# Performance work log

Measured on AMD Instinct MI355X. Metric: run time of the kernel, lower is better.

The kernel has to match this reference:

```python
import jax, jax.numpy as jnp
import numpy as np

N = 100000
E = 1600000
D_IN = 128
H = 128
C = 3
EPS_BN = 1e-5
EPS_LN = 1e-5


def _gcn_conv(x, W, b, src, dst, ew, n):
    # PyG GCNConv: x' = D^{-1/2} (A + I) D^{-1/2} (x W) + b, self-loop weight 1
    x = x @ W
    loop = jnp.arange(n)
    src2 = jnp.concatenate([src, loop])
    dst2 = jnp.concatenate([dst, loop])
    ew2 = jnp.concatenate([ew, jnp.ones((n,), dtype=x.dtype)])
    deg = jax.ops.segment_sum(ew2, dst2, num_segments=n)
    dinv = jnp.where(deg > 0, jax.lax.rsqrt(jnp.maximum(deg, 1e-12)), 0.0)
    norm = dinv[src2] * ew2 * dinv[dst2]  # [E+N]
    msgs = x[src2] * norm[:, None]        # [E+N, H] gathered messages
    out = jax.ops.segment_sum(msgs, dst2, num_segments=n)
    return out + b


def setup_inputs() -> dict:
    key = jax.random.key(0)
    ks = jax.random.split(key, 16)
    def lin(k, i, o):
        s = 1.0 / np.sqrt(i)
        k1, k2 = jax.random.split(k)
        return (jax.random.uniform(k1, (i, o), jnp.float32, -s, s),
                jax.random.uniform(k2, (o,), jnp.float32, -s, s))
    x = jax.random.normal(ks[0], (N, D_IN), jnp.float32)
    edge_index = jax.random.randint(ks[1], (2, E), 0, N, jnp.int64)
    edge_attr = jax.random.uniform(ks[2], (E, 1), jnp.float32)
    W_pre, b_pre = lin(ks[3], D_IN, H)
    W1, b1 = lin(ks[4], H, H)
    W2, b2 = lin(ks[5], H, H)
    Wc1, bc1 = lin(ks[6], H, H)
    Wc2, bc2 = lin(ks[7], H, C)
    return {
        "x": x, "edge_index": edge_index, "edge_attr": edge_attr,
        "W_pre": W_pre, "b_pre": b_pre,
        "bn_gamma": jnp.ones((H,), jnp.float32), "bn_beta": jnp.zeros((H,), jnp.float32),
        "bn_mean": jnp.zeros((H,), jnp.float32), "bn_var": jnp.ones((H,), jnp.float32),
        "W1": W1, "b1": b1, "W2": W2, "b2": b2,
        "Wc1": Wc1, "bc1": bc1,
        "ln_g": jnp.ones((H,), jnp.float32), "ln_b": jnp.zeros((H,), jnp.float32),
        "Wc2": Wc2, "bc2": bc2,
    }


def reference(x, edge_index, edge_attr, W_pre, b_pre, bn_gamma, bn_beta, bn_mean, bn_var,
              W1, b1, W2, b2, Wc1, bc1, ln_g, ln_b, Wc2, bc2):
    src, dst = edge_index[0], edge_index[1]
    ew = edge_attr.squeeze()
    n = x.shape[0]
    # input_preprocess: Linear -> BatchNorm1d (eval: running stats) -> ReLU (dropout=identity)
    h = x @ W_pre + b_pre
    h = (h - bn_mean) * jax.lax.rsqrt(bn_var + EPS_BN) * bn_gamma + bn_beta
    h = jax.nn.relu(h)
    residual = h
    # conv layer 1 (+ ReLU, dropout identity in eval)
    h = jax.nn.relu(_gcn_conv(h, W1, b1, src, dst, ew, n))
    # conv layer 2 (last: no activation)
    h = _gcn_conv(h, W2, b2, src, dst, ew, n)
    h = h + residual  # shapes match
    # classifier: Linear -> LayerNorm -> ReLU -> (dropout) -> Linear
    z = h @ Wc1 + bc1
    mu = jnp.mean(z, axis=-1, keepdims=True)
    var = jnp.mean((z - mu) ** 2, axis=-1, keepdims=True)
    z = (z - mu) * jax.lax.rsqrt(var + EPS_LN) * ln_g + ln_b
    z = jax.nn.relu(z)
    return z @ Wc2 + bc2
```

## Files before the change

kernel.cpp:

```cpp
#include <hip/hip_runtime.h>
#include <hip/hip_bf16.h>

typedef __bf16 bf16_t;
typedef bf16_t bf16x8 __attribute__((ext_vector_type(8)));
typedef bf16_t bf16x4 __attribute__((ext_vector_type(4)));
typedef float f32x4 __attribute__((ext_vector_type(4)));
typedef float f32x2 __attribute__((ext_vector_type(2)));

#define EPS_BN 1e-5f
#define EPS_LN 1e-5f
#define SLOTS 32
#define WSCALE 32767.f
#define WINV (1.f / 32767.f)
#define RNODES 448
#define OV_CAP 16384
#define OVA_CAP 65536

__device__ __forceinline__ float blo(unsigned u) { return __uint_as_float(u << 16); }
__device__ __forceinline__ float bhi(unsigned u) { return __uint_as_float(u & 0xFFFF0000u); }
__device__ __forceinline__ f32x2 f8lo(unsigned u) { return __builtin_amdgcn_cvt_pk_f32_fp8((int)u, false); }
__device__ __forceinline__ f32x2 f8hi(unsigned u) { return __builtin_amdgcn_cvt_pk_f32_fp8((int)u, true); }


__global__ void prepK(const float* __restrict__ W0, const float* __restrict__ W1,
                      const float* __restrict__ W2, const float* __restrict__ W3,
                      bf16_t* __restrict__ WT, int* __restrict__ bCnt,
                      int* __restrict__ ovCnt, int* __restrict__ ovACnt, int n) {
    int flat = blockIdx.x * 256 + threadIdx.x;
    if (flat == 0) { *ovCnt = 0; *ovACnt = 0; }
    if (flat < 4096) bCnt[flat] = 0;
    if (flat < 65536) {
        int which = flat >> 14, r = flat & 16383;
        const float* W = (which == 0) ? W0 : (which == 1) ? W1 : (which == 2) ? W2 : W3;
        int i = r >> 7, o = r & 127;
        WT[which * 128 * 136 + o * 136 + i] = (bf16_t)W[r];
    }
}


__global__ __launch_bounds__(256) void binK(
    const int* __restrict__ ei, const float* __restrict__ ea,
    uint2* __restrict__ bbuf, int* __restrict__ bCnt,
    uint2* __restrict__ ovA, int* __restrict__ ovACnt,
    int E, int cap, int nbuck)
{
    __shared__ int lcnt[256];
    __shared__ int gbase[256];
    int tid = threadIdx.x;
    if (tid < nbuck) lcnt[tid] = 0;
    __syncthreads();

    int e0 = blockIdx.x * 4096 + tid;
    int d[16]; unsigned pk[16]; int p[16];
#pragma unroll
    for (int k = 0; k < 16; ++k) {
        int e = e0 + k * 256;
        p[k] = -1;
        if (e < E) {
            d[k] = ei[E + e];
            int s = ei[e];
            unsigned wq = __float2uint_rn(ea[e] * WSCALE);
            pk[k] = ((unsigned)s << 15) | wq;
            p[k] = atomicAdd(&lcnt[(unsigned)d[k] / RNODES], 1);
        }
    }
    __syncthreads();
    if (tid < nbuck) gbase[tid] = atomicAdd(&bCnt[tid * 16], lcnt[tid]);
    __syncthreads();
#pragma unroll
    for (int k = 0; k < 16; ++k) {
        if (p[k] >= 0) {
            int b = (unsigned)d[k] / RNODES;
            int idx = gbase[b] + p[k];
            if (idx < cap) {
                bbuf[(size_t)b * cap + idx] = make_uint2((unsigned)d[k], pk[k]);
            } else {
                int o = atomicAdd(ovACnt, 1);
                if (o < OVA_CAP) ovA[o] = make_uint2((unsigned)d[k], pk[k]);
            }
        }
    }
}


__global__ __launch_bounds__(256) void buildK(
    const uint2* __restrict__ bbuf, const int* __restrict__ bCnt,
    const uint2* __restrict__ ovA, const int* __restrict__ ovACnt,
    unsigned* __restrict__ slots, int* __restrict__ cnt,
    float* __restrict__ dinv, uint2* __restrict__ ov, int* __restrict__ ovCnt,
    int cap, int n)
{
    __shared__ unsigned slotsL[RNODES * 32];
    __shared__ int cntL[RNODES];
    __shared__ float wsumL[RNODES];
    int tid = threadIdx.x;
    int base = blockIdx.x * RNODES;

    for (int j = tid; j < RNODES; j += 256) { cntL[j] = 0; wsumL[j] = 0.f; }
    __syncthreads();

    int nb = min(bCnt[blockIdx.x * 16], cap);
    const uint2* buf = bbuf + (size_t)blockIdx.x * cap;
    for (int i = tid; i < nb; i += 256) {
        uint2 u = buf[i];
        int local = (int)u.x - base;
        int pos = atomicAdd(&cntL[local], 1);
        atomicAdd(&wsumL[local], (float)(u.y & 32767u) * WINV);
        if (pos < SLOTS) {
            slotsL[local * 32 + pos] = u.y;
        } else {
            int o = atomicAdd(ovCnt, 1);
            if (o < OV_CAP) ov[o] = u;
        }
    }
    int no = min(*ovACnt, OVA_CAP);
    for (int k = tid; k < no; k += 256) {
        uint2 u = ovA[k];
        int local = (int)u.x - base;
        if (local >= 0 && local < RNODES) {
            int pos = atomicAdd(&cntL[local], 1);
            atomicAdd(&wsumL[local], (float)(u.y & 32767u) * WINV);
            if (pos < SLOTS) {
                slotsL[local * 32 + pos] = u.y;
            } else {
                int o = atomicAdd(ovCnt, 1);
                if (o < OV_CAP) ov[o] = u;
            }
        }
    }
    __syncthreads();

    for (int j = tid; j < RNODES; j += 256) {
        int node = base + j;
        if (node < n) {
            int c = cntL[j];
            int cm = min(c, SLOTS);
            int c8 = (cm + 7) & ~7;
            for (int k2 = cm; k2 < c8; ++k2) slotsL[j * 32 + k2] = (unsigned)node << 15;
            cnt[node] = c;
            dinv[node] = rsqrtf(fmaxf(1.f + wsumL[j], 1e-12f));
        }
    }
    __syncthreads();

    int vnodes = min(n - base, RNODES);
    if (vnodes <= 0) return;
    const uint4* sl4 = (const uint4*)slotsL;
    uint4* sg4 = (uint4*)(slots + ((size_t)base << 5));
    int lim = vnodes * 8;
    for (int i = tid; i < lim; i += 256) sg4[i] = sl4[i];
}


template <int MODE, typename AT>
__global__ __launch_bounds__(256) void gemm128K(
    const AT* __restrict__ A, const bf16_t* __restrict__ WT,
    bf16_t* __restrict__ outb, unsigned* __restrict__ out8,
    const float* __restrict__ colBias,
    const float* __restrict__ bnMean, const float* __restrict__ bnVar,
    const float* __restrict__ bnG, const float* __restrict__ bnB,
    const float* __restrict__ dinv, int nrows)
{
    __shared__ __align__(16) bf16_t Bs[128 * 136];
    int tid = threadIdx.x;
    int rb = blockIdx.x * 64;

    {
        const uint4* src = (const uint4*)WT;
        uint4* dst = (uint4*)Bs;
        if (MODE == 1) {
            for (int i = tid; i < 128 * 17; i += 256) {
                int row = i / 17, k = i - row * 17;
                int so = ((row & 15) << 3) | (row >> 4);
                dst[row * 17 + k] = src[so * 17 + k];
            }
        } else {
            for (int i = tid; i < 128 * 17; i += 256) dst[i] = src[i];
        }
    }

    int lane = tid & 63;
    int wid = tid >> 6;
    int m = lane & 15, q = lane >> 4;
    int myRow = rb + wid * 16 + m;
    int rowL = min(myRow, nrows - 1);

    bf16x8 af[4];
    if constexpr (sizeof(AT) == 4) {
#pragma unroll
        for (int kk = 0; kk < 4; ++kk) {
            float4 v0 = ((const float4*)A)[rowL * 32 + q * 2 + kk * 8];
            float4 v1 = ((const float4*)A)[rowL * 32 + q * 2 + kk * 8 + 1];
            bf16x8 w8;
            w8[0] = (bf16_t)v0.x; w8[1] = (bf16_t)v0.y; w8[2] = (bf16_t)v0.z; w8[3] = (bf16_t)v0.w;
            w8[4] = (bf16_t)v1.x; w8[5] = (bf16_t)v1.y; w8[6] = (bf16_t)v1.z; w8[7] = (bf16_t)v1.w;
            af[kk] = w8;
        }
    } else {
#pragma unroll
        for (int kk = 0; kk < 4; ++kk)
            af[kk] = ((const bf16x8*)A)[rowL * 16 + q + kk * 4];
    }

    __syncthreads();

    f32x4 acc[8];
#pragma unroll
    for (int c = 0; c < 8; ++c) acc[c] = (f32x4){0.f, 0.f, 0.f, 0.f};

#pragma unroll
    for (int kk = 0; kk < 4; ++kk) {
#pragma unroll
        for (int c = 0; c < 8; ++c) {
            bf16x8 bfr = *(const bf16x8*)&Bs[(c * 16 + m) * 136 + q * 8 + kk * 32];
            acc[c] = __builtin_amdgcn_mfma_f32_16x16x32_bf16(af[kk], bfr, acc[c], 0, 0, 0);
        }
    }

    int r0 = rb + wid * 16 + q * 4;
    if (MODE == 1) {
        float dv[4];
#pragma unroll
        for (int i = 0; i < 4; ++i) dv[i] = (r0 + i < nrows) ? dinv[r0 + i] : 0.f;
#pragma unroll
        for (int i = 0; i < 4; ++i) {
            int r = r0 + i;
            if (r < nrows) {
                float v0 = acc[0][i] * dv[i], v1 = acc[1][i] * dv[i];
                float v2 = acc[2][i] * dv[i], v3 = acc[3][i] * dv[i];
                float v4 = acc[4][i] * dv[i], v5 = acc[5][i] * dv[i];
                float v6 = acc[6][i] * dv[i], v7 = acc[7][i] * dv[i];
                int lo = __builtin_amdgcn_cvt_pk_fp8_f32(v0, v1, 0, false);
                lo = __builtin_amdgcn_cvt_pk_fp8_f32(v2, v3, lo, true);
                int hi = __builtin_amdgcn_cvt_pk_fp8_f32(v4, v5, 0, false);
                hi = __builtin_amdgcn_cvt_pk_fp8_f32(v6, v7, hi, true);
                ((uint2*)out8)[(r << 4) | m] = make_uint2((unsigned)lo, (unsigned)hi);
            }
        }
    } else {
#pragma unroll
        for (int c = 0; c < 8; ++c) {
            int j = c * 16 + m;
            float cb = colBias[j];
            float rs = rsqrtf(bnVar[j] + EPS_BN);
            float scale = bnG[j] * rs;
            float shift = bnB[j] - bnMean[j] * scale;
#pragma unroll
            for (int i = 0; i < 4; ++i) {
                int r = r0 + i;
                if (r < nrows) {
                    float v = (acc[c][i] + cb) * scale + shift;
                    outb[r * 128 + j] = (bf16_t)fmaxf(v, 0.f);
                }
            }
        }
    }
}


template <int RELU, int RES>
__global__ __launch_bounds__(256) void aggK(
    const uint4* __restrict__ ts16, const unsigned* __restrict__ slots,
    const int* __restrict__ cnt, const float* __restrict__ dinv,
    const float4* __restrict__ bias, const uint4* __restrict__ residual,
    uint4* __restrict__ out,
    const uint2* __restrict__ ov, const int* __restrict__ ovCnt, int n)
{
    int tid = threadIdx.x;
    int node = blockIdx.x * 8 + (tid >> 5);
    int hl = tid & 31;
    int hb = tid & 32;
    if (node >= n) return;
    int slot = hl >> 3;
    int f = hl & 7;
    int nb = node << 5;

    int c8 = (min(cnt[node], SLOTS) + 7) & ~7;
    unsigned my = slots[nb | hl];
    float myw = (float)(my & 32767u) * WINV;
    int myoff = (int)(my >> 15) << 3;

    f32x2 acc[8];
#pragma unroll
    for (int k = 0; k < 8; ++k) acc[k] = (f32x2){0.f, 0.f};

    if (slot == 1) {
        uint4 su = ts16[(node << 3) + f];
        acc[0] += f8lo(su.x); acc[1] += f8hi(su.x);
        acc[2] += f8lo(su.y); acc[3] += f8hi(su.y);
        acc[4] += f8lo(su.z); acc[5] += f8hi(su.z);
        acc[6] += f8lo(su.w); acc[7] += f8hi(su.w);
    }

    for (int j = 0; j < c8; j += 8) {
        int s0 = hb + j + slot;
        int s1 = s0 + 4;
        int o0 = __shfl(myoff, s0);
        int o1 = __shfl(myoff, s1);
        float w0 = __shfl(myw, s0);
        float w1 = __shfl(myw, s1);
        uint4 u0 = ts16[o0 + f];
        uint4 u1 = ts16[o1 + f];
        f32x2 W0 = (f32x2){w0, w0}, W1 = (f32x2){w1, w1};
        acc[0] += W0 * f8lo(u0.x) + W1 * f8lo(u1.x);
        acc[1] += W0 * f8hi(u0.x) + W1 * f8hi(u1.x);
        acc[2] += W0 * f8lo(u0.y) + W1 * f8lo(u1.y);
        acc[3] += W0 * f8hi(u0.y) + W1 * f8hi(u1.y);
        acc[4] += W0 * f8lo(u0.z) + W1 * f8lo(u1.z);
        acc[5] += W0 * f8hi(u0.z) + W1 * f8hi(u1.z);
        acc[6] += W0 * f8lo(u0.w) + W1 * f8lo(u1.w);
        acc[7] += W0 * f8hi(u0.w) + W1 * f8hi(u1.w);
    }

    int no = min(*ovCnt, OV_CAP);
    for (int k = 0; k < no; ++k) {
        uint2 o = ov[k];
        if ((int)o.x == node && slot == 0) {
            uint4 u = ts16[((int)(o.y >> 15) << 3) + f];
            float w = (float)(o.y & 32767u) * WINV;
            f32x2 W = (f32x2){w, w};
            acc[0] += W * f8lo(u.x); acc[1] += W * f8hi(u.x);
            acc[2] += W * f8lo(u.y); acc[3] += W * f8hi(u.y);
            acc[4] += W * f8lo(u.z); acc[5] += W * f8hi(u.z);
            acc[6] += W * f8lo(u.w); acc[7] += W * f8hi(u.w);
        }
    }

#pragma unroll
    for (int k = 0; k < 8; ++k) {
        f32x2 t;
        t.x = __shfl_xor(acc[k].x, 8);  t.y = __shfl_xor(acc[k].y, 8);
        acc[k] += t;
        t.x = __shfl_xor(acc[k].x, 16); t.y = __shfl_xor(acc[k].y, 16);
        acc[k] += t;
    }

    if (slot == 0) {
        float di = dinv[node];
        float r[16];
#pragma unroll
        for (int k = 0; k < 8; ++k) {
            float4 bb = bias[f * 4 + (k >> 1)];
            float b0 = (k & 1) ? bb.z : bb.x;
            float b1 = (k & 1) ? bb.w : bb.y;
            r[2 * k]     = acc[k].x * di + b0;
            r[2 * k + 1] = acc[k].y * di + b1;
        }
        if (RES) {
            uint4 q0 = residual[(node << 4) + f * 2];
            uint4 q1 = residual[(node << 4) + f * 2 + 1];
            r[0] += blo(q0.x);  r[1] += bhi(q0.x);
            r[2] += blo(q0.y);  r[3] += bhi(q0.y);
            r[4] += blo(q0.z);  r[5] += bhi(q0.z);
            r[6] += blo(q0.w);  r[7] += bhi(q0.w);
            r[8] += blo(q1.x);  r[9] += bhi(q1.x);
            r[10] += blo(q1.y); r[11] += bhi(q1.y);
            r[12] += blo(q1.z); r[13] += bhi(q1.z);
            r[14] += blo(q1.w); r[15] += bhi(q1.w);
        }
        if (RELU) {
#pragma unroll
            for (int k = 0; k < 16; ++k) r[k] = fmaxf(r[k], 0.f);
        }
        bf16x8 o0, o1;
#pragma unroll
        for (int k = 0; k < 8; ++k) { o0[k] = (bf16_t)r[k]; o1[k] = (bf16_t)r[8 + k]; }
        out[(node << 4) + f * 2]     = *(uint4*)&o0;
        out[(node << 4) + f * 2 + 1] = *(uint4*)&o1;
    }
}


__global__ __launch_bounds__(256) void classifierK(
    const bf16_t* __restrict__ A, const bf16_t* __restrict__ WT,
    const float* __restrict__ bc1, const float* __restrict__ g,
    const float* __restrict__ b, const float* __restrict__ Wc2,
    const float* __restrict__ bc2, float* __restrict__ out, int nrows)
{
    __shared__ __align__(16) bf16_t Bs[128 * 136];
    __shared__ float sB[128], sG[128], sLb[128], sW2[384];
    int tid = threadIdx.x;
    int rb = blockIdx.x * 64;

    {
        const uint4* src = (const uint4*)WT;
        uint4* dst = (uint4*)Bs;
        for (int i = tid; i < 128 * 17; i += 256) dst[i] = src[i];
    }
    if (tid < 128) { sB[tid] = bc1[tid]; sG[tid] = g[tid]; sLb[tid] = b[tid]; }
    for (int i = tid; i < 384; i += 256) sW2[i] = Wc2[i];

    int lane = tid & 63;
    int wid = tid >> 6;
    int m = lane & 15, q = lane >> 4;
    int rowL = min(rb + wid * 16 + m, nrows - 1);

    bf16x8 af[4];
#pragma unroll
    for (int kk = 0; kk < 4; ++kk)
        af[kk] = ((const bf16x8*)A)[rowL * 16 + q + kk * 4];

    __syncthreads();

    f32x4 acc[8];
#pragma unroll
    for (int c = 0; c < 8; ++c) acc[c] = (f32x4){0.f, 0.f, 0.f, 0.f};
#pragma unroll
    for (int kk = 0; kk < 4; ++kk) {
#pragma unroll
        for (int c = 0; c < 8; ++c) {
            bf16x8 bfr = *(const bf16x8*)&Bs[(c * 16 + m) * 136 + q * 8 + kk * 32];
            acc[c] = __builtin_amdgcn_mfma_f32_16x16x32_bf16(af[kk], bfr, acc[c], 0, 0, 0);
        }
    }

    int r0 = rb + wid * 16 + q * 4;
#pragma unroll
    for (int i = 0; i < 4; ++i) {
        float s1 = 0.f, s2 = 0.f;
#pragma unroll
        for (int c = 0; c < 8; ++c) {
            float z = acc[c][i] + sB[c * 16 + m];
            acc[c][i] = z;
            s1 += z; s2 += z * z;
        }
#pragma unroll
        for (int off = 1; off < 16; off <<= 1) {
            s1 += __shfl_xor(s1, off);
            s2 += __shfl_xor(s2, off);
        }
        float mu = s1 * (1.f / 128.f);
        float var = s2 * (1.f / 128.f) - mu * mu;
        float rstd = rsqrtf(var + EPS_LN);
        float p0 = 0.f, p1 = 0.f, p2 = 0.f;
#pragma unroll
        for (int c = 0; c < 8; ++c) {
            int j = c * 16 + m;
            float zn = (acc[c][i] - mu) * rstd * sG[j] + sLb[j];
            zn = fmaxf(zn, 0.f);
            p0 += zn * sW2[j * 3 + 0];
            p1 += zn * sW2[j * 3 + 1];
            p2 += zn * sW2[j * 3 + 2];
        }
#pragma unroll
        for (int off = 1; off < 16; off <<= 1) {
            p0 += __shfl_xor(p0, off);
            p1 += __shfl_xor(p1, off);
            p2 += __shfl_xor(p2, off);
        }
        int r = r0 + i;
        if (m == 0 && r < nrows) {
            out[r * 3 + 0] = p0 + bc2[0];
            out[r * 3 + 1] = p1 + bc2[1];
            out[r * 3 + 2] = p2 + bc2[2];
        }
    }
}


extern "C" void kernel_launch(void* const* d_in, const int* in_sizes, int n_in,
                              void* d_out, int out_size, void* d_ws, size_t ws_size,
                              hipStream_t stream) {
    const float* x      = (const float*)d_in[0];
    const int*   ei     = (const int*)d_in[1];
    const float* ea     = (const float*)d_in[2];
    const float* W_pre  = (const float*)d_in[3];
    const float* b_pre  = (const float*)d_in[4];
    const float* bn_g   = (const float*)d_in[5];
    const float* bn_b   = (const float*)d_in[6];
    const float* bn_m   = (const float*)d_in[7];
    const float* bn_v   = (const float*)d_in[8];
    const float* W1     = (const float*)d_in[9];
    const float* b1     = (const float*)d_in[10];
    const float* W2     = (const float*)d_in[11];
    const float* b2     = (const float*)d_in[12];
    const float* Wc1    = (const float*)d_in[13];
    const float* bc1    = (const float*)d_in[14];
    const float* ln_g   = (const float*)d_in[15];
    const float* ln_b   = (const float*)d_in[16];
    const float* Wc2    = (const float*)d_in[17];
    const float* bc2    = (const float*)d_in[18];
    float* outp = (float*)d_out;

    const int N = in_sizes[0] / 128;
    const int E = in_sizes[2];

    char* p = (char*)d_ws;
    auto alloc = [&](size_t bytes) -> void* {
        void* r = (void*)p;
        p += (bytes + 255) & ~(size_t)255;
        return r;
    };
    bf16_t*   h0    = (bf16_t*)alloc((size_t)N * 128 * 2);
    bf16_t*   bufB  = (bf16_t*)alloc((size_t)N * 128 * 2);
    unsigned* ts8   = (unsigned*)alloc((size_t)N * 128);
    float*    dinv  = (float*)alloc((size_t)N * 4);
    int*      cnt   = (int*)alloc((size_t)N * 4);
    int*      ovCnt = (int*)alloc(256);
    int*      ovACnt= (int*)alloc(256);
    uint2*    ov    = (uint2*)alloc((size_t)OV_CAP * 8);
    uint2*    ovA   = (uint2*)alloc((size_t)OVA_CAP * 8);
    unsigned* slots = (unsigned*)alloc((size_t)N * SLOTS * 4);
    bf16_t*   WT    = (bf16_t*)alloc((size_t)4 * 128 * 136 * 2);
    int       nbuck = (N + RNODES - 1) / RNODES;
    int       cap   = E / nbuck + 4096;
    uint2*    bbuf  = (uint2*)alloc((size_t)nbuck * cap * 8);
    int*      bCnt  = (int*)alloc(4096 * 4);

    bf16_t* WT_pre = WT + 0 * 128 * 136;
    bf16_t* WT_1   = WT + 1 * 128 * 136;
    bf16_t* WT_2   = WT + 2 * 128 * 136;
    bf16_t* WT_c1  = WT + 3 * 128 * 136;

    int gG = (N + 63) / 64;
    int gH = (N + 7) / 8;
    int gP = (max(N, 65536) + 255) / 256;
    int gBin = (E + 4095) / 4096;

    prepK<<<gP, 256, 0, stream>>>(W_pre, W1, W2, Wc1, WT, bCnt, ovCnt, ovACnt, N);
    binK<<<gBin, 256, 0, stream>>>(ei, ea, bbuf, bCnt, ovA, ovACnt, E, cap, nbuck);
    buildK<<<nbuck, 256, 0, stream>>>(bbuf, bCnt, ovA, ovACnt, slots, cnt, dinv, ov, ovCnt, cap, N);

    gemm128K<0, float><<<gG, 256, 0, stream>>>(x, WT_pre, h0, nullptr, b_pre, bn_m, bn_v, bn_g, bn_b, nullptr, N);
    gemm128K<1, bf16_t><<<gG, 256, 0, stream>>>(h0, WT_1, nullptr, ts8, nullptr, nullptr, nullptr, nullptr, nullptr, dinv, N);
    aggK<1, 0><<<gH, 256, 0, stream>>>((const uint4*)ts8, slots, cnt, dinv, (const float4*)b1,
                                       nullptr, (uint4*)bufB, ov, ovCnt, N);
    gemm128K<1, bf16_t><<<gG, 256, 0, stream>>>(bufB, WT_2, nullptr, ts8, nullptr, nullptr, nullptr, nullptr, nullptr, dinv, N);
    aggK<0, 1><<<gH, 256, 0, stream>>>((const uint4*)ts8, slots, cnt, dinv, (const float4*)b2,
                                       (const uint4*)h0, (uint4*)bufB, ov, ovCnt, N);
    classifierK<<<gG, 256, 0, stream>>>(bufB, WT_c1, bc1, ln_g, ln_b, Wc2, bc2, outp, N);
}
```

Baseline: 322.4 us.

## Persistent GEMM blocks and software-pipelined neighbor gathers in aggregation

The GEMM and classifier kernels become grid-stride persistent loops capped at 1024 blocks. Each block now loads the 128x128 weight tile into shared memory once and reuses it across many row groups, instead of reloading it for every 64 rows. The aggregation kernel double-buffers its neighbor gathers: it prefetches the next pair of fp8 rows and their weights before accumulating the current pair, which hides gather latency at the cost of extra registers. It also loads the self-row unconditionally and trims the prepK launch size.

```diff
diff --git a/kernel.cpp b/kernel.cpp
--- a/kernel.cpp
+++ b/kernel.cpp
@@ -25,7 +25,7 @@
 __global__ void prepK(const float* __restrict__ W0, const float* __restrict__ W1,
                       const float* __restrict__ W2, const float* __restrict__ W3,
                       bf16_t* __restrict__ WT, int* __restrict__ bCnt,
-                      int* __restrict__ ovCnt, int* __restrict__ ovACnt, int n) {
+                      int* __restrict__ ovCnt, int* __restrict__ ovACnt) {
     int flat = blockIdx.x * 256 + threadIdx.x;
     if (flat == 0) { *ovCnt = 0; *ovACnt = 0; }
     if (flat < 4096) bCnt[flat] = 0;
@@ -86,8 +86,8 @@
 __global__ __launch_bounds__(256) void buildK(
     const uint2* __restrict__ bbuf, const int* __restrict__ bCnt,
     const uint2* __restrict__ ovA, const int* __restrict__ ovACnt,
-    unsigned* __restrict__ slots, int* __restrict__ cnt,
-    float* __restrict__ dinv, uint2* __restrict__ ov, int* __restrict__ ovCnt,
+    unsigned* __restrict__ slots, int* __restrict__ cnt, float* __restrict__ dinv,
+    uint2* __restrict__ ov, int* __restrict__ ovCnt,
     int cap, int n)
 {
     __shared__ unsigned slotsL[RNODES * 32];
@@ -159,11 +159,10 @@
     const float* __restrict__ colBias,
     const float* __restrict__ bnMean, const float* __restrict__ bnVar,
     const float* __restrict__ bnG, const float* __restrict__ bnB,
-    const float* __restrict__ dinv, int nrows)
+    const float* __restrict__ dinv, int nrows, int ngroups)
 {
     __shared__ __align__(16) bf16_t Bs[128 * 136];
     int tid = threadIdx.x;
-    int rb = blockIdx.x * 64;
 
     {
         const uint4* src = (const uint4*)WT;
@@ -182,81 +181,99 @@
     int lane = tid & 63;
     int wid = tid >> 6;
     int m = lane & 15, q = lane >> 4;
-    int myRow = rb + wid * 16 + m;
-    int rowL = min(myRow, nrows - 1);
-
-    bf16x8 af[4];
-    if constexpr (sizeof(AT) == 4) {
-#pragma unroll
-        for (int kk = 0; kk < 4; ++kk) {
-            float4 v0 = ((const float4*)A)[rowL * 32 + q * 2 + kk * 8];
-            float4 v1 = ((const float4*)A)[rowL * 32 + q * 2 + kk * 8 + 1];
-            bf16x8 w8;
-            w8[0] = (bf16_t)v0.x; w8[1] = (bf16_t)v0.y; w8[2] = (bf16_t)v0.z; w8[3] = (bf16_t)v0.w;
-            w8[4] = (bf16_t)v1.x; w8[5] = (bf16_t)v1.y; w8[6] = (bf16_t)v1.z; w8[7] = (bf16_t)v1.w;
-            af[kk] = w8;
-        }
-    } else {
-#pragma unroll
-        for (int kk = 0; kk < 4; ++kk)
-            af[kk] = ((const bf16x8*)A)[rowL * 16 + q + kk * 4];
-    }
-
-    __syncthreads();
-
-    f32x4 acc[8];
-#pragma unroll
-    for (int c = 0; c < 8; ++c) acc[c] = (f32x4){0.f, 0.f, 0.f, 0.f};
-
-#pragma unroll
-    for (int kk = 0; kk < 4; ++kk) {
-#pragma unroll
-        for (int c = 0; c < 8; ++c) {
-            bf16x8 bfr = *(const bf16x8*)&Bs[(c * 16 + m) * 136 + q * 8 + kk * 32];
-            acc[c] = __builtin_amdgcn_mfma_f32_16x16x32_bf16(af[kk], bfr, acc[c], 0, 0, 0);
-        }
-    }
-
-    int r0 = rb + wid * 16 + q * 4;
-    if (MODE == 1) {
-        float dv[4];
-#pragma unroll
-        for (int i = 0; i < 4; ++i) dv[i] = (r0 + i < nrows) ? dinv[r0 + i] : 0.f;
-#pragma unroll
-        for (int i = 0; i < 4; ++i) {
-            int r = r0 + i;
-            if (r < nrows) {
-                float v0 = acc[0][i] * dv[i], v1 = acc[1][i] * dv[i];
-                float v2 = acc[2][i] * dv[i], v3 = acc[3][i] * dv[i];
-                float v4 = acc[4][i] * dv[i], v5 = acc[5][i] * dv[i];
-                float v6 = acc[6][i] * dv[i], v7 = acc[7][i] * dv[i];
-                int lo = __builtin_amdgcn_cvt_pk_fp8_f32(v0, v1, 0, false);
-                lo = __builtin_amdgcn_cvt_pk_fp8_f32(v2, v3, lo, true);
-                int hi = __builtin_amdgcn_cvt_pk_fp8_f32(v4, v5, 0, false);
-                hi = __builtin_amdgcn_cvt_pk_fp8_f32(v6, v7, hi, true);
-                ((uint2*)out8)[(r << 4) | m] = make_uint2((unsigned)lo, (unsigned)hi);
-            }
-        }
-    } else {
+
+    float cb[8], scale[8], shift[8];
+    if (MODE == 0) {
 #pragma unroll
         for (int c = 0; c < 8; ++c) {
             int j = c * 16 + m;
-            float cb = colBias[j];
+            cb[c] = colBias[j];
             float rs = rsqrtf(bnVar[j] + EPS_BN);
-            float scale = bnG[j] * rs;
-            float shift = bnB[j] - bnMean[j] * scale;
+            scale[c] = bnG[j] * rs;
+            shift[c] = bnB[j] - bnMean[j] * scale[c];
+        }
+    }
+
+    __syncthreads();
+
+    for (int g = blockIdx.x; g < ngroups; g += gridDim.x) {
+        int rb = g * 64;
+        int myRow = rb + wid * 16 + m;
+        int rowL = min(myRow, nrows - 1);
+
+        bf16x8 af[4];
+        if constexpr (sizeof(AT) == 4) {
+#pragma unroll
+            for (int kk = 0; kk < 4; ++kk) {
+                float4 v0 = ((const float4*)A)[rowL * 32 + q * 2 + kk * 8];
+                float4 v1 = ((const float4*)A)[rowL * 32 + q * 2 + kk * 8 + 1];
+                bf16x8 w8;
+                w8[0] = (bf16_t)v0.x; w8[1] = (bf16_t)v0.y; w8[2] = (bf16_t)v0.z; w8[3] = (bf16_t)v0.w;
+                w8[4] = (bf16_t)v1.x; w8[5] = (bf16_t)v1.y; w8[6] = (bf16_t)v1.z; w8[7] = (bf16_t)v1.w;
+                af[kk] = w8;
+            }
+        } else {
+#pragma unroll
+            for (int kk = 0; kk < 4; ++kk)
+                af[kk] = ((const bf16x8*)A)[rowL * 16 + q + kk * 4];
+        }
+
+        f32x4 acc[8];
+#pragma unroll
+        for (int c = 0; c < 8; ++c) acc[c] = (f32x4){0.f, 0.f, 0.f, 0.f};
+
+#pragma unroll
+        for (int kk = 0; kk < 4; ++kk) {
+#pragma unroll
+            for (int c = 0; c < 8; ++c) {
+                bf16x8 bfr = *(const bf16x8*)&Bs[(c * 16 + m) * 136 + q * 8 + kk * 32];
+                acc[c] = __builtin_amdgcn_mfma_f32_16x16x32_bf16(af[kk], bfr, acc[c], 0, 0, 0);
+            }
+        }
+
+        int r0 = rb + wid * 16 + q * 4;
+        if (MODE == 1) {
+            float dv[4];
+#pragma unroll
+            for (int i = 0; i < 4; ++i) dv[i] = (r0 + i < nrows) ? dinv[r0 + i] : 0.f;
 #pragma unroll
             for (int i = 0; i < 4; ++i) {
                 int r = r0 + i;
                 if (r < nrows) {
-                    float v = (acc[c][i] + cb) * scale + shift;
-                    outb[r * 128 + j] = (bf16_t)fmaxf(v, 0.f);
+                    float v0 = acc[0][i] * dv[i], v1 = acc[1][i] * dv[i];
+                    float v2 = acc[2][i] * dv[i], v3 = acc[3][i] * dv[i];
+                    float v4 = acc[4][i] * dv[i], v5 = acc[5][i] * dv[i];
+                    float v6 = acc[6][i] * dv[i], v7 = acc[7][i] * dv[i];
+                    int lo = __builtin_amdgcn_cvt_pk_fp8_f32(v0, v1, 0, false);
+                    lo = __builtin_amdgcn_cvt_pk_fp8_f32(v2, v3, lo, true);
+                    int hi = __builtin_amdgcn_cvt_pk_fp8_f32(v4, v5, 0, false);
+                    hi = __builtin_amdgcn_cvt_pk_fp8_f32(v6, v7, hi, true);
+                    ((uint2*)out8)[(r << 4) | m] = make_uint2((unsigned)lo, (unsigned)hi);
                 }
             }
-        }
-    }
-}
-
+        } else {
+#pragma unroll
+            for (int c = 0; c < 8; ++c) {
+#pragma unroll
+                for (int i = 0; i < 4; ++i) {
+                    int r = r0 + i;
+                    if (r < nrows) {
+                        float v = (acc[c][i] + cb[c]) * scale[c] + shift[c];
+                        outb[r * 128 + (c * 16 + m)] = (bf16_t)fmaxf(v, 0.f);
+                    }
+                }
+            }
+        }
+    }
+}
+
+
+#define ACC8(U, W) do { \
+    f32x2 Wv = (f32x2){(W), (W)}; \
+    acc[0] += Wv * f8lo((U).x); acc[1] += Wv * f8hi((U).x); \
+    acc[2] += Wv * f8lo((U).y); acc[3] += Wv * f8hi((U).y); \
+    acc[4] += Wv * f8lo((U).z); acc[5] += Wv * f8hi((U).z); \
+    acc[6] += Wv * f8lo((U).w); acc[7] += Wv * f8hi((U).w); } while (0)
 
 template <int RELU, int RES>
 __global__ __launch_bounds__(256) void aggK(
@@ -273,56 +290,57 @@
     if (node >= n) return;
     int slot = hl >> 3;
     int f = hl & 7;
-    int nb = node << 5;
 
     int c8 = (min(cnt[node], SLOTS) + 7) & ~7;
-    unsigned my = slots[nb | hl];
+    int nit = c8 >> 3;
+    unsigned my = slots[(node << 5) | hl];
     float myw = (float)(my & 32767u) * WINV;
     int myoff = (int)(my >> 15) << 3;
 
+    uint4 su = ts16[(node << 3) + f];
+
+    int s0 = hb + slot;
+    int po0 = __shfl(myoff, s0);
+    int po1 = __shfl(myoff, s0 + 4);
+    float pw0 = __shfl(myw, s0);
+    float pw1 = __shfl(myw, s0 + 4);
+    uint4 u0 = su, u1 = su;
+    if (nit > 0) { u0 = ts16[po0 + f]; u1 = ts16[po1 + f]; }
+
     f32x2 acc[8];
 #pragma unroll
     for (int k = 0; k < 8; ++k) acc[k] = (f32x2){0.f, 0.f};
 
     if (slot == 1) {
-        uint4 su = ts16[(node << 3) + f];
         acc[0] += f8lo(su.x); acc[1] += f8hi(su.x);
         acc[2] += f8lo(su.y); acc[3] += f8hi(su.y);
         acc[4] += f8lo(su.z); acc[5] += f8hi(su.z);
         acc[6] += f8lo(su.w); acc[7] += f8hi(su.w);
     }
 
-    for (int j = 0; j < c8; j += 8) {
-        int s0 = hb + j + slot;
-        int s1 = s0 + 4;
-        int o0 = __shfl(myoff, s0);
-        int o1 = __shfl(myoff, s1);
-        float w0 = __shfl(myw, s0);
-        float w1 = __shfl(myw, s1);
-        uint4 u0 = ts16[o0 + f];
-        uint4 u1 = ts16[o1 + f];
-        f32x2 W0 = (f32x2){w0, w0}, W1 = (f32x2){w1, w1};
-        acc[0] += W0 * f8lo(u0.x) + W1 * f8lo(u1.x);
-        acc[1] += W0 * f8hi(u0.x) + W1 * f8hi(u1.x);
-        acc[2] += W0 * f8lo(u0.y) + W1 * f8lo(u1.y);
-        acc[3] += W0 * f8hi(u0.y) + W1 * f8hi(u1.y);
-        acc[4] += W0 * f8lo(u0.z) + W1 * f8lo(u1.z);
-        acc[5] += W0 * f8hi(u0.z) + W1 * f8hi(u1.z);
-        acc[6] += W0 * f8lo(u0.w) + W1 * f8lo(u1.w);
-        acc[7] += W0 * f8hi(u0.w) + W1 * f8hi(u1.w);
+    for (int j = 0; j < nit; ++j) {
+        uint4 v0 = u0, v1 = u1;
+        float x0 = pw0, x1 = pw1;
+        if (j + 1 < nit) {
+            int s = hb + (j + 1) * 8 + slot;
+            int no0 = __shfl(myoff, s);
+            int no1 = __shfl(myoff, s + 4);
+            pw0 = __shfl(myw, s);
+            pw1 = __shfl(myw, s + 4);
+            u0 = ts16[no0 + f];
+            u1 = ts16[no1 + f];
+        }
+        ACC8(v0, x0);
+        ACC8(v1, x1);
     }
 
     int no = min(*ovCnt, OV_CAP);
     for (int k = 0; k < no; ++k) {
-        uint2 o = ov[k];
-        if ((int)o.x == node && slot == 0) {
-            uint4 u = ts16[((int)(o.y >> 15) << 3) + f];
-            float w = (float)(o.y & 32767u) * WINV;
-            f32x2 W = (f32x2){w, w};
-            acc[0] += W * f8lo(u.x); acc[1] += W * f8hi(u.x);
-            acc[2] += W * f8lo(u.y); acc[3] += W * f8hi(u.y);
-            acc[4] += W * f8lo(u.z); acc[5] += W * f8hi(u.z);
-            acc[6] += W * f8lo(u.w); acc[7] += W * f8hi(u.w);
+        uint2 ovk = ov[k];
+        if ((int)ovk.x == node && slot == 0) {
+            uint4 uo = ts16[((int)(ovk.y >> 15) << 3) + f];
+            float wo = (float)(ovk.y & 32767u) * WINV;
+            ACC8(uo, wo);
         }
     }
 
@@ -375,12 +393,11 @@
     const bf16_t* __restrict__ A, const bf16_t* __restrict__ WT,
     const float* __restrict__ bc1, const float* __restrict__ g,
     const float* __restrict__ b, const float* __restrict__ Wc2,
-    const float* __restrict__ bc2, float* __restrict__ out, int nrows)
+    const float* __restrict__ bc2, float* __restrict__ out, int nrows, int ngroups)
 {
     __shared__ __align__(16) bf16_t Bs[128 * 136];
     __shared__ float sB[128], sG[128], sLb[128], sW2[384];
     int tid = threadIdx.x;
-    int rb = blockIdx.x * 64;
 
     {
         const uint4* src = (const uint4*)WT;
@@ -393,66 +410,70 @@
     int lane = tid & 63;
     int wid = tid >> 6;
     int m = lane & 15, q = lane >> 4;
-    int rowL = min(rb + wid * 16 + m, nrows - 1);
-
-    bf16x8 af[4];
-#pragma unroll
-    for (int kk = 0; kk < 4; ++kk)
-        af[kk] = ((const bf16x8*)A)[rowL * 16 + q + kk * 4];
-
-    __syncthreads();
-
-    f32x4 acc[8];
-#pragma unroll
-    for (int c = 0; c < 8; ++c) acc[c] = (f32x4){0.f, 0.f, 0.f, 0.f};
-#pragma unroll
-    for (int kk = 0; kk < 4; ++kk) {
-#pragma unroll
-        for (int c = 0; c < 8; ++c) {
-            bf16x8 bfr = *(const bf16x8*)&Bs[(c * 16 + m) * 136 + q * 8 + kk * 32];
-            acc[c] = __builtin_amdgcn_mfma_f32_16x16x32_bf16(af[kk], bfr, acc[c], 0, 0, 0);
-        }
-    }
-
-    int r0 = rb + wid * 16 + q * 4;
-#pragma unroll
-    for (int i = 0; i < 4; ++i) {
-        float s1 = 0.f, s2 = 0.f;
-#pragma unroll
-        for (int c = 0; c < 8; ++c) {
-            float z = acc[c][i] + sB[c * 16 + m];
-            acc[c][i] = z;
-            s1 += z; s2 += z * z;
-        }
-#pragma unroll
-        for (int off = 1; off < 16; off <<= 1) {
-            s1 += __shfl_xor(s1, off);
-            s2 += __shfl_xor(s2, off);
-        }
-        float mu = s1 * (1.f / 128.f);
-        float var = s2 * (1.f / 128.f) - mu * mu;
-        float rstd = rsqrtf(var + EPS_LN);
-        float p0 = 0.f, p1 = 0.f, p2 = 0.f;
-#pragma unroll
-        for (int c = 0; c < 8; ++c) {
-            int j = c * 16 + m;
-            float zn = (acc[c][i] - mu) * rstd * sG[j] + sLb[j];
-            zn = fmaxf(zn, 0.f);
-            p0 += zn * sW2[j * 3 + 0];
-            p1 += zn * sW2[j * 3 + 1];
-            p2 += zn * sW2[j * 3 + 2];
-        }
-#pragma unroll
-        for (int off = 1; off < 16; off <<= 1) {
-            p0 += __shfl_xor(p0, off);
-            p1 += __shfl_xor(p1, off);
-            p2 += __shfl_xor(p2, off);
-        }
-        int r = r0 + i;
-        if (m == 0 && r < nrows) {
-            out[r * 3 + 0] = p0 + bc2[0];
-            out[r * 3 + 1] = p1 + bc2[1];
-            out[r * 3 + 2] = p2 + bc2[2];
+
+    __syncthreads();
+
+    for (int grp = blockIdx.x; grp < ngroups; grp += gridDim.x) {
+        int rb = grp * 64;
+        int rowL = min(rb + wid * 16 + m, nrows - 1);
+
+        bf16x8 af[4];
+#pragma unroll
+        for (int kk = 0; kk < 4; ++kk)
+            af[kk] = ((const bf16x8*)A)[rowL * 16 + q + kk * 4];
+
+        f32x4 acc[8];
+#pragma unroll
+        for (int c = 0; c < 8; ++c) acc[c] = (f32x4){0.f, 0.f, 0.f, 0.f};
+#pragma unroll
+        for (int kk = 0; kk < 4; ++kk) {
+#pragma unroll
+            for (int c = 0; c < 8; ++c) {
+                bf16x8 bfr = *(const bf16x8*)&Bs[(c * 16 + m) * 136 + q * 8 + kk * 32];
+                acc[c] = __builtin_amdgcn_mfma_f32_16x16x32_bf16(af[kk], bfr, acc[c], 0, 0, 0);
+            }
+        }
+
+        int r0 = rb + wid * 16 + q * 4;
+#pragma unroll
+        for (int i = 0; i < 4; ++i) {
+            float s1 = 0.f, s2 = 0.f;
+#pragma unroll
+            for (int c = 0; c < 8; ++c) {
+                float z = acc[c][i] + sB[c * 16 + m];
+                acc[c][i] = z;
+                s1 += z; s2 += z * z;
+            }
+#pragma unroll
+            for (int off = 1; off < 16; off <<= 1) {
+                s1 += __shfl_xor(s1, off);
+                s2 += __shfl_xor(s2, off);
+            }
+            float mu = s1 * (1.f / 128.f);
+            float var = s2 * (1.f / 128.f) - mu * mu;
+            float rstd = rsqrtf(var + EPS_LN);
+            float p0 = 0.f, p1 = 0.f, p2 = 0.f;
+#pragma unroll
+            for (int c = 0; c < 8; ++c) {
+                int j = c * 16 + m;
+                float zn = (acc[c][i] - mu) * rstd * sG[j] + sLb[j];
+                zn = fmaxf(zn, 0.f);
+                p0 += zn * sW2[j * 3 + 0];
+                p1 += zn * sW2[j * 3 + 1];
+                p2 += zn * sW2[j * 3 + 2];
+            }
+#pragma unroll
+            for (int off = 1; off < 16; off <<= 1) {
+                p0 += __shfl_xor(p0, off);
+                p1 += __shfl_xor(p1, off);
+                p2 += __shfl_xor(p2, off);
+            }
+            int r = r0 + i;
+            if (m == 0 && r < nrows) {
+                out[r * 3 + 0] = p0 + bc2[0];
+                out[r * 3 + 1] = p1 + bc2[1];
+                out[r * 3 + 2] = p2 + bc2[2];
+            }
         }
     }
 }
@@ -513,20 +534,21 @@
     bf16_t* WT_c1  = WT + 3 * 128 * 136;
 
     int gG = (N + 63) / 64;
+    int nBlk = gG < 1024 ? gG : 1024;
     int gH = (N + 7) / 8;
-    int gP = (max(N, 65536) + 255) / 256;
+    int gP = 65536 / 256;
     int gBin = (E + 4095) / 4096;
 
-    prepK<<<gP, 256, 0, stream>>>(W_pre, W1, W2, Wc1, WT, bCnt, ovCnt, ovACnt, N);
+    prepK<<<gP, 256, 0, stream>>>(W_pre, W1, W2, Wc1, WT, bCnt, ovCnt, ovACnt);
     binK<<<gBin, 256, 0, stream>>>(ei, ea, bbuf, bCnt, ovA, ovACnt, E, cap, nbuck);
     buildK<<<nbuck, 256, 0, stream>>>(bbuf, bCnt, ovA, ovACnt, slots, cnt, dinv, ov, ovCnt, cap, N);
 
-    gemm128K<0, float><<<gG, 256, 0, stream>>>(x, WT_pre, h0, nullptr, b_pre, bn_m, bn_v, bn_g, bn_b, nullptr, N);
-    gemm128K<1, bf16_t><<<gG, 256, 0, stream>>>(h0, WT_1, nullptr, ts8, nullptr, nullptr, nullptr, nullptr, nullptr, dinv, N);
+    gemm128K<0, float><<<nBlk, 256, 0, stream>>>(x, WT_pre, h0, nullptr, b_pre, bn_m, bn_v, bn_g, bn_b, nullptr, N, gG);
+    gemm128K<1, bf16_t><<<nBlk, 256, 0, stream>>>(h0, WT_1, nullptr, ts8, nullptr, nullptr, nullptr, nullptr, nullptr, dinv, N, gG);
     aggK<1, 0><<<gH, 256, 0, stream>>>((const uint4*)ts8, slots, cnt, dinv, (const float4*)b1,
                                        nullptr, (uint4*)bufB, ov, ovCnt, N);
-    gemm128K<1, bf16_t><<<gG, 256, 0, stream>>>(bufB, WT_2, nullptr, ts8, nullptr, nullptr, nullptr, nullptr, nullptr, dinv, N);
+    gemm128K<1, bf16_t><<<nBlk, 256, 0, stream>>>(bufB, WT_2, nullptr, ts8, nullptr, nullptr, nullptr, nullptr, nullptr, dinv, N, gG);
     aggK<0, 1><<<gH, 256, 0, stream>>>((const uint4*)ts8, slots, cnt, dinv, (const float4*)b2,
                                        (const uint4*)h0, (uint4*)bufB, ov, ovCnt, N);
-    classifierK<<<gG, 256, 0, stream>>>(bufB, WT_c1, bc1, ln_g, ln_b, Wc2, bc2, outp, N);
-}
+    classifierK<<<nBlk, 256, 0, stream>>>(bufB, WT_c1, bc1, ln_g, ln_b, Wc2, bc2, outp, N, gG);
+}
```

New measurement: 341.1 us. +5.8%, slower.
